# Performance work log

Measured on AMD Instinct MI355X. Metric: run time of the kernel, lower is better.

Reference implementation:

```python
import jax, jax.numpy as jnp
import numpy as np

K = 32          # neighbors
HEAD_DIM = 8    # out_channels // num_heads = 64 // 8


def _ln(x, g, b, eps=1e-5):
    m = x.mean(-1, keepdims=True)
    v = ((x - m) ** 2).mean(-1, keepdims=True)
    return (x - m) * jax.lax.rsqrt(v + eps) * g + b


def _knn(x, k):
    # x: [B,N,3]; torch code takes top-k of NEGATIVE squared distance -> nearest
    sq = jnp.sum(x * x, axis=-1)                        # [B,N]
    inner = jnp.einsum('bnc,bmc->bnm', x, x)            # [B,N,N]
    neg_dist = -(sq[:, :, None] - 2.0 * inner + sq[:, None, :])
    return jax.lax.top_k(neg_dist, k)[1]                # [B,N,k]


def _gather(points, idx):
    # points: [B,M,C], idx: [B,N,K] -> [B,N,K,C]
    return jax.vmap(lambda p, i: p[i])(points, idx)


def _forward(xyz, features, ln1_g, ln1_b, Wq, bq, Wk, bk, Wv, bv,
             d_W1, d_b1, d_g, d_b, d_W2, d_b2,
             g_W1, g_b1, g_g, g_b, g_W2, g_b2,
             Wo, bo, ln2_g, ln2_b, ca_W1, ca_b1, ca_W2, ca_b2, ln3_g, ln3_b):
    fn = _ln(features, ln1_g, ln1_b)                    # norm1
    idx = _knn(xyz, K)                                  # [B,N,K]
    nxyz = _gather(xyz, idx)                            # [B,N,K,3]
    nfeat = _gather(fn, idx)                            # [B,N,K,C]
    pos_diff = xyz[:, :, None, :] - nxyz                # [B,N,K,3]
    # fc_delta: Linear -> LN -> ReLU -> Linear
    pe = jax.nn.relu(_ln(pos_diff @ d_W1 + d_b1, d_g, d_b)) @ d_W2 + d_b2
    q = (fn @ Wq + bq)[:, :, None, :]                   # [B,N,1,C]
    k = nfeat @ Wk + bk                                 # [B,N,K,C]
    v = nfeat @ Wv + bv
    # head permutes in torch are identity reshapes; vector attention in [B,N,K,C]
    attn_in = q - k + pe
    a = jax.nn.relu(_ln(attn_in @ g_W1 + g_b1, g_g, g_b)) @ g_W2 + g_b2
    a = jax.nn.softmax(a / np.sqrt(HEAD_DIM).astype(np.float32), axis=2)
    out = jnp.sum(a * (v + pe), axis=2)                 # [B,N,C]
    out = _ln(out @ Wo + bo, ln2_g, ln2_b)              # fc_out + norm2
    cw = jax.nn.sigmoid(jax.nn.relu(out.mean(axis=1) @ ca_W1 + ca_b1) @ ca_W2 + ca_b2)
    out = _ln(out * cw[:, None, :], ln3_g, ln3_b)       # channel attn + norm3
    return out + features                               # in==out -> no skip_proj


def setup_inputs() -> dict:
    key = jax.random.key(0)
    ks = jax.random.split(key, 12)
    B, N, C = 2, 8192, 64
    s = 1.0 / np.sqrt(C)
    w = lambda k, shape, sc: jax.random.normal(k, shape, jnp.float32) * sc
    return dict(
        xyz=jax.random.normal(ks[0], (B, N, 3), jnp.float32),
        features=jax.random.normal(ks[1], (B, N, C), jnp.float32),
        ln1_g=jnp.ones(C), ln1_b=jnp.zeros(C),
        Wq=w(ks[2], (C, C), s), bq=jnp.zeros(C),
        Wk=w(ks[3], (C, C), s), bk=jnp.zeros(C),
        Wv=w(ks[4], (C, C), s), bv=jnp.zeros(C),
        d_W1=w(ks[5], (3, C), 1.0 / np.sqrt(3)), d_b1=jnp.zeros(C),
        d_g=jnp.ones(C), d_b=jnp.zeros(C),
        d_W2=w(ks[6], (C, C), s), d_b2=jnp.zeros(C),
        g_W1=w(ks[7], (C, C), s), g_b1=jnp.zeros(C),
        g_g=jnp.ones(C), g_b=jnp.zeros(C),
        g_W2=w(ks[8], (C, C), s), g_b2=jnp.zeros(C),
        Wo=w(ks[9], (C, C), s), bo=jnp.zeros(C),
        ln2_g=jnp.ones(C), ln2_b=jnp.zeros(C),
        ca_W1=w(ks[10], (C, C // 4), s), ca_b1=jnp.zeros(C // 4),
        ca_W2=w(ks[11], (C // 4, C), 1.0 / np.sqrt(C // 4)), ca_b2=jnp.zeros(C),
        ln3_g=jnp.ones(C), ln3_b=jnp.zeros(C),
    )


def reference(xyz, features, ln1_g, ln1_b, Wq, bq, Wk, bk, Wv, bv,
              d_W1, d_b1, d_g, d_b, d_W2, d_b2,
              g_W1, g_b1, g_g, g_b, g_W2, g_b2,
              Wo, bo, ln2_g, ln2_b, ca_W1, ca_b1, ca_W2, ca_b2, ln3_g, ln3_b):
    return _forward(xyz, features, ln1_g, ln1_b, Wq, bq, Wk, bk, Wv, bv,
                    d_W1, d_b1, d_g, d_b, d_W2, d_b2,
                    g_W1, g_b1, g_g, g_b, g_W2, g_b2,
                    Wo, bo, ln2_g, ln2_b, ca_W1, ca_b1, ca_W2, ca_b2, ln3_g, ln3_b)
```

## Files before the change

### kernel.cpp

```cpp
#include <hip/hip_runtime.h>

static constexpr int gB = 2;
static constexpr int gN = 8192;
static constexpr int gC = 64;
static constexpr int gK = 32;

using u16 = unsigned short;
using u32 = unsigned int;
using u64 = unsigned long long;

__device__ __forceinline__ float wsum(float v) {
#pragma unroll
    for (int m = 32; m; m >>= 1) v += __shfl_xor(v, m, 64);
    return v;
}

__device__ __forceinline__ u16 f2bf(float f) {
    u32 u = __float_as_uint(f);
    return (u16)((u + 0x7FFFu + ((u >> 16) & 1u)) >> 16);
}
__device__ __forceinline__ float bf2f(u16 v) {
    return __uint_as_float(((u32)v) << 16);
}

__global__ __launch_bounds__(256) void k_lnqkv(
    const float* __restrict__ feat, const float* __restrict__ ln1g, const float* __restrict__ ln1b,
    const float* __restrict__ Wq, const float* __restrict__ bq,
    const float* __restrict__ Wk, const float* __restrict__ bk,
    const float* __restrict__ Wv, const float* __restrict__ bv,
    float* __restrict__ Qo, float* __restrict__ Ko, float* __restrict__ Vo,
    float* __restrict__ zero_region)
{
    if (blockIdx.x == 0) zero_region[threadIdx.x] = 0.f;
    int wave = threadIdx.x >> 6, lane = threadIdx.x & 63;
    int p = blockIdx.x * 4 + wave;
    float x = feat[(size_t)p * gC + lane];
    float mu = wsum(x) * (1.f / 64);
    float d = x - mu;
    float var = wsum(d * d) * (1.f / 64);
    float inv = 1.f / sqrtf(var + 1e-5f);
    float fn = d * inv * ln1g[lane] + ln1b[lane];
    float qa = bq[lane], ka = bk[lane], va = bv[lane];
    for (int cp = 0; cp < 64; ++cp) {
        float hv = __shfl(fn, cp, 64);
        qa += hv * Wq[cp * 64 + lane];
        ka += hv * Wk[cp * 64 + lane];
        va += hv * Wv[cp * 64 + lane];
    }
    size_t o = (size_t)p * gC + lane;
    Qo[o] = qa; Ko[o] = ka; Vo[o] = va;
}

__global__ __launch_bounds__(64) void k_knn(const float* __restrict__ xyz, int* __restrict__ idxo)
{
#pragma clang fp contract(off)
    int lane = threadIdx.x;
    int q = blockIdx.x;
    int b = q >> 13;
    int n = q & (gN - 1);
    const float* base = xyz + (size_t)b * gN * 3;
    float xi = base[n * 3 + 0];
    float yi = base[n * 3 + 1];
    float zi = base[n * 3 + 2];
    float ni_ = sqrtf((xi * xi + yi * yi) + zi * zi);
    float sqi = ni_ * ni_;
    u64 lst[10];
#pragma unroll
    for (int e = 0; e < 10; ++e) lst[e] = 0ull;
    for (int jj = 0; jj < 128; ++jj) {
        int j = (jj << 6) | lane;
        float x = base[j * 3 + 0];
        float y = base[j * 3 + 1];
        float z = base[j * 3 + 2];
        float nj_ = sqrtf((x * x + y * y) + z * z);
        float sqj = nj_ * nj_;
        float inner = (xi * x + yi * y) + zi * z;
        float nd = -((sqi - 2.0f * inner) + sqj);
        u32 u = __float_as_uint(nd);
        u32 kh = u ^ (0x80000000u | (u32)((int)u >> 31));
        u64 pk = ((u64)kh << 32) | (u32)(8191 - j);
        if (pk > lst[9]) {
            lst[9] = pk;
#pragma unroll
            for (int e = 9; e > 0; --e) {
                if (lst[e] > lst[e - 1]) { u64 t = lst[e - 1]; lst[e - 1] = lst[e]; lst[e] = t; }
            }
        }
    }
    int* op = idxo + (size_t)q * gK;
    for (int r = 0; r < gK; ++r) {
        u64 g = lst[0];
#pragma unroll
        for (int m = 32; m; m >>= 1) {
            u64 o = __shfl_xor(g, m, 64);
            g = (o > g) ? o : g;
        }
        if (lst[0] == g) {
#pragma unroll
            for (int e = 0; e < 9; ++e) lst[e] = lst[e + 1];
            lst[9] = 0ull;
        }
        if (lane == 0) op[r] = 8191 - (int)(g & 0x1FFFu);
    }
}

__global__ __launch_bounds__(64, 2) void k_attn(
    const float* __restrict__ xyz,
    const float* __restrict__ Qb, const float* __restrict__ Kb, const float* __restrict__ Vb,
    const int* __restrict__ idxi,
    const float* __restrict__ dW1, const float* __restrict__ db1,
    const float* __restrict__ dgv, const float* __restrict__ dbv,
    const float* __restrict__ dW2, const float* __restrict__ db2,
    const float* __restrict__ gW1, const float* __restrict__ gb1,
    const float* __restrict__ ggv, const float* __restrict__ gbv,
    const float* __restrict__ gW2, const float* __restrict__ gb2,
    float* __restrict__ att)
{
    __shared__ u16 actb[64][64];
    __shared__ u16 peb[64][64];
    __shared__ float qlds[2][64];
    int lane = threadIdx.x;
    int half = lane >> 5;
    int kk = lane & 31;
    int pA = blockIdx.x * 2;
    int p = pA + half;
    int b = p >> 13;

    qlds[0][lane] = Qb[(size_t)pA * gC + lane];
    qlds[1][lane] = Qb[(size_t)(pA + 1) * gC + lane];
    __syncthreads();

    int j = idxi[(size_t)p * gK + kk];
    const float* xp = xyz + (size_t)p * 3;
    const float* xj = xyz + ((size_t)b * gN + j) * 3;
    float dx = xp[0] - xj[0];
    float dy = xp[1] - xj[1];
    float dz = xp[2] - xj[2];

    float acc[64];

#pragma unroll
    for (int c = 0; c < 64; ++c)
        acc[c] = dx * dW1[c] + dy * dW1[64 + c] + dz * dW1[128 + c] + db1[c];

    {
        float s0 = 0, s1 = 0, s2 = 0, s3 = 0;
#pragma unroll
        for (int c = 0; c < 64; c += 4) { s0 += acc[c]; s1 += acc[c + 1]; s2 += acc[c + 2]; s3 += acc[c + 3]; }
        float mu = ((s0 + s1) + (s2 + s3)) * (1.f / 64);
        float v0 = 0, v1 = 0, v2 = 0, v3 = 0;
#pragma unroll
        for (int c = 0; c < 64; c += 4) {
            acc[c] -= mu; acc[c + 1] -= mu; acc[c + 2] -= mu; acc[c + 3] -= mu;
            v0 += acc[c] * acc[c]; v1 += acc[c + 1] * acc[c + 1];
            v2 += acc[c + 2] * acc[c + 2]; v3 += acc[c + 3] * acc[c + 3];
        }
        float var = ((v0 + v1) + (v2 + v3)) * (1.f / 64);
        float inv = 1.f / sqrtf(var + 1e-5f);
#pragma unroll
        for (int c = 0; c < 64; ++c)
            actb[c][lane] = f2bf(fmaxf(acc[c] * inv * dgv[c] + dbv[c], 0.f));
    }

#pragma unroll
    for (int c = 0; c < 64; ++c) acc[c] = db2[c];
    for (int cp = 0; cp < 64; ++cp) {
        float h = bf2f(actb[cp][lane]);
#pragma unroll
        for (int c = 0; c < 64; ++c) acc[c] += h * dW2[cp * 64 + c];
    }
#pragma unroll
    for (int c = 0; c < 64; ++c) peb[c][lane] = f2bf(acc[c]);

    {
        const float* Kj = Kb + ((size_t)b * gN + j) * gC;
#pragma unroll
        for (int c4 = 0; c4 < 16; ++c4) {
            float4 kv = reinterpret_cast<const float4*>(Kj)[c4];
            int c = c4 * 4;
            actb[c + 0][lane] = f2bf((qlds[half][c + 0] - kv.x) + acc[c + 0]);
            actb[c + 1][lane] = f2bf((qlds[half][c + 1] - kv.y) + acc[c + 1]);
            actb[c + 2][lane] = f2bf((qlds[half][c + 2] - kv.z) + acc[c + 2]);
            actb[c + 3][lane] = f2bf((qlds[half][c + 3] - kv.w) + acc[c + 3]);
        }
    }

#pragma unroll
    for (int c = 0; c < 64; ++c) acc[c] = gb1[c];
    for (int cp = 0; cp < 64; ++cp) {
        float h = bf2f(actb[cp][lane]);
#pragma unroll
        for (int c = 0; c < 64; ++c) acc[c] += h * gW1[cp * 64 + c];
    }
    {
        float s0 = 0, s1 = 0, s2 = 0, s3 = 0;
#pragma unroll
        for (int c = 0; c < 64; c += 4) { s0 += acc[c]; s1 += acc[c + 1]; s2 += acc[c + 2]; s3 += acc[c + 3]; }
        float mu = ((s0 + s1) + (s2 + s3)) * (1.f / 64);
        float v0 = 0, v1 = 0, v2 = 0, v3 = 0;
#pragma unroll
        for (int c = 0; c < 64; c += 4) {
            acc[c] -= mu; acc[c + 1] -= mu; acc[c + 2] -= mu; acc[c + 3] -= mu;
            v0 += acc[c] * acc[c]; v1 += acc[c + 1] * acc[c + 1];
            v2 += acc[c + 2] * acc[c + 2]; v3 += acc[c + 3] * acc[c + 3];
        }
        float var = ((v0 + v1) + (v2 + v3)) * (1.f / 64);
        float inv = 1.f / sqrtf(var + 1e-5f);
#pragma unroll
        for (int c = 0; c < 64; ++c)
            actb[c][lane] = f2bf(fmaxf(acc[c] * inv * ggv[c] + gbv[c], 0.f));
    }

#pragma unroll
    for (int c = 0; c < 64; ++c) acc[c] = gb2[c];
    for (int cp = 0; cp < 64; ++cp) {
        float h = bf2f(actb[cp][lane]);
#pragma unroll
        for (int c = 0; c < 64; ++c) acc[c] += h * gW2[cp * 64 + c];
    }
#pragma unroll
    for (int c = 0; c < 64; ++c)
        acc[c] = acc[c] * 0.3535533905932738f;

    {
        const float* Vj = Vb + ((size_t)b * gN + j) * gC;
        float* op = att + (size_t)p * gC;
        for (int c4 = 0; c4 < 16; ++c4) {
            float4 vv4 = reinterpret_cast<const float4*>(Vj)[c4];
            float vva[4] = {vv4.x, vv4.y, vv4.z, vv4.w};
#pragma unroll
            for (int i = 0; i < 4; ++i) {
                int c = c4 * 4 + i;
                float l = acc[c];
                float gm = l;
#pragma unroll
                for (int m = 16; m; m >>= 1) gm = fmaxf(gm, __shfl_xor(gm, m, 64));
                float e = expf(l - gm);
                float w = e * (vva[i] + bf2f(peb[c][lane]));
                float se = e, sw = w;
#pragma unroll
                for (int m = 16; m; m >>= 1) {
                    se += __shfl_xor(se, m, 64);
                    sw += __shfl_xor(sw, m, 64);
                }
                if (kk == (c & 31)) op[c] = sw / se;
            }
        }
    }
}

__global__ __launch_bounds__(256) void k_out(
    float* __restrict__ att,
    const float* __restrict__ Wo, const float* __restrict__ bo,
    const float* __restrict__ ln2g, const float* __restrict__ ln2b,
    float* __restrict__ meanb)
{
    __shared__ __align__(16) float hb[4][64];
    int lane = threadIdx.x & 63;
    int p = blockIdx.x * 4 + (threadIdx.x >> 6);
    int b = p >> 13;
    float* hbuf = hb[threadIdx.x >> 6];
    float wo[64];
#pragma unroll
    for (int r = 0; r < 64; ++r) wo[r] = Wo[r * 64 + lane];
    float x = att[(size_t)p * gC + lane];
    hbuf[lane] = x;
    float acc = bo[lane];
#pragma unroll
    for (int q4 = 0; q4 < 16; ++q4) {
        float4 hq = *reinterpret_cast<const float4*>(&hbuf[q4 * 4]);
        acc += hq.x * wo[q4 * 4 + 0] + hq.y * wo[q4 * 4 + 1]
             + hq.z * wo[q4 * 4 + 2] + hq.w * wo[q4 * 4 + 3];
    }
    float mu = wsum(acc) * (1.f / 64);
    float d = acc - mu;
    float var = wsum(d * d) * (1.f / 64);
    float inv = 1.f / sqrtf(var + 1e-5f);
    float y = d * inv * ln2g[lane] + ln2b[lane];
    att[(size_t)p * gC + lane] = y;
    atomicAdd(&meanb[b * 64 + lane], y * (1.f / gN));
}

__global__ void k_cw(const float* __restrict__ meanb,
                     const float* __restrict__ caW1, const float* __restrict__ cab1,
                     const float* __restrict__ caW2, const float* __restrict__ cab2,
                     float* __restrict__ cw)
{
    int b = blockIdx.x, lane = threadIdx.x;
    float mv = meanb[b * 64 + lane];
    float hj = (lane < 16) ? cab1[lane] : 0.f;
    for (int cp = 0; cp < 64; ++cp) {
        float mcp = __shfl(mv, cp, 64);
        if (lane < 16) hj += mcp * caW1[cp * 16 + lane];
    }
    hj = fmaxf(hj, 0.f);
    float acc = cab2[lane];
    for (int jj = 0; jj < 16; ++jj) {
        float hv = __shfl(hj, jj, 64);
        acc += hv * caW2[jj * 64 + lane];
    }
    cw[b * 64 + lane] = 1.f / (1.f + expf(-acc));
}

__global__ __launch_bounds__(256) void k_final(
    const float* __restrict__ out2, const float* __restrict__ cw,
    const float* __restrict__ ln3g, const float* __restrict__ ln3b,
    const float* __restrict__ feat, float* __restrict__ outp)
{
    int lane = threadIdx.x & 63;
    int p = blockIdx.x * 4 + (threadIdx.x >> 6);
    int b = p >> 13;
    float x = out2[(size_t)p * gC + lane] * cw[b * 64 + lane];
    float mu = wsum(x) * (1.f / 64);
    float d = x - mu;
    float var = wsum(d * d) * (1.f / 64);
    float inv = 1.f / sqrtf(var + 1e-5f);
    float y = d * inv * ln3g[lane] + ln3b[lane];
    outp[(size_t)p * gC + lane] = y + feat[(size_t)p * gC + lane];
}

extern "C" void kernel_launch(void* const* d_in, const int* in_sizes, int n_in,
                              void* d_out, int out_size, void* d_ws, size_t ws_size,
                              hipStream_t stream)
{
    (void)in_sizes; (void)n_in; (void)out_size; (void)ws_size;
    const float* xyz  = (const float*)d_in[0];
    const float* feat = (const float*)d_in[1];
    const float* ln1g = (const float*)d_in[2];
    const float* ln1b = (const float*)d_in[3];
    const float* Wq   = (const float*)d_in[4];
    const float* bq   = (const float*)d_in[5];
    const float* Wk   = (const float*)d_in[6];
    const float* bk   = (const float*)d_in[7];
    const float* Wv   = (const float*)d_in[8];
    const float* bv   = (const float*)d_in[9];
    const float* dW1  = (const float*)d_in[10];
    const float* db1  = (const float*)d_in[11];
    const float* dg   = (const float*)d_in[12];
    const float* db   = (const float*)d_in[13];
    const float* dW2  = (const float*)d_in[14];
    const float* db2  = (const float*)d_in[15];
    const float* gW1  = (const float*)d_in[16];
    const float* gb1  = (const float*)d_in[17];
    const float* gg   = (const float*)d_in[18];
    const float* gb   = (const float*)d_in[19];
    const float* gW2  = (const float*)d_in[20];
    const float* gb2  = (const float*)d_in[21];
    const float* Wo   = (const float*)d_in[22];
    const float* bo   = (const float*)d_in[23];
    const float* ln2g = (const float*)d_in[24];
    const float* ln2b = (const float*)d_in[25];
    const float* caW1 = (const float*)d_in[26];
    const float* cab1 = (const float*)d_in[27];
    const float* caW2 = (const float*)d_in[28];
    const float* cab2 = (const float*)d_in[29];
    const float* ln3g = (const float*)d_in[30];
    const float* ln3b = (const float*)d_in[31];

    const size_t BNC = (size_t)gB * gN * gC;
    float* Q    = (float*)d_ws;
    float* Kt   = Q + BNC;
    float* Vt   = Kt + BNC;
    float* att  = Vt + BNC;
    int*   idx  = (int*)(att + BNC);
    float* meanb = (float*)(idx + (size_t)gB * gN * gK);
    float* cw    = meanb + 128;

    const int PB = (gB * gN) / 4;

    k_lnqkv<<<PB, 256, 0, stream>>>(feat, ln1g, ln1b, Wq, bq, Wk, bk, Wv, bv, Q, Kt, Vt, meanb);
    k_knn<<<gB * gN, 64, 0, stream>>>(xyz, idx);
    k_attn<<<(gB * gN) / 2, 64, 0, stream>>>(xyz, Q, Kt, Vt, idx,
                                             dW1, db1, dg, db, dW2, db2,
                                             gW1, gb1, gg, gb, gW2, gb2, att);
    k_out<<<PB, 256, 0, stream>>>(att, Wo, bo, ln2g, ln2b, meanb);
    k_cw<<<gB, 64, 0, stream>>>(meanb, caW1, cab1, caW2, cab2, cw);
    k_final<<<PB, 256, 0, stream>>>(att, cw, ln3g, ln3b, feat, (float*)d_out);
}
```

Measured before the change: 1.178 ms.

## Remap attention kernel to lane-per-channel with LDS-staged bf16 weights

```diff
diff --git a/kernel.cpp b/kernel.cpp
--- a/kernel.cpp
+++ b/kernel.cpp
@@ -104,7 +104,7 @@
     }
 }
 
-__global__ __launch_bounds__(64, 2) void k_attn(
+__global__ __launch_bounds__(256, 2) void k_attn(
     const float* __restrict__ xyz,
     const float* __restrict__ Qb, const float* __restrict__ Kb, const float* __restrict__ Vb,
     const int* __restrict__ idxi,
@@ -116,136 +116,133 @@
     const float* __restrict__ gW2, const float* __restrict__ gb2,
     float* __restrict__ att)
 {
-    __shared__ u16 actb[64][64];
-    __shared__ u16 peb[64][64];
-    __shared__ float qlds[2][64];
-    int lane = threadIdx.x;
-    int half = lane >> 5;
-    int kk = lane & 31;
-    int pA = blockIdx.x * 2;
-    int p = pA + half;
+    __shared__ u16 wd2s[64 * 64];
+    __shared__ u16 wg1s[64 * 64];
+    __shared__ u16 wg2s[64 * 64];
+    __shared__ float hbuf[4][32][64];
+    __shared__ u16 pebuf[4][32][64];
+    __shared__ float4 dxb[4][32];
+    __shared__ int jb[4][32];
+
+    int tid = threadIdx.x;
+    int w = tid >> 6, lane = tid & 63;
+    int p = blockIdx.x * 4 + w;
     int b = p >> 13;
 
-    qlds[0][lane] = Qb[(size_t)pA * gC + lane];
-    qlds[1][lane] = Qb[(size_t)(pA + 1) * gC + lane];
+    for (int i = tid; i < 4096; i += 256) {
+        int cp = i >> 6, c = i & 63;
+        int di = c * 64 + ((((cp >> 2) ^ (c & 15)) << 2) | (cp & 3));
+        wd2s[di] = f2bf(dW2[i]);
+        wg1s[di] = f2bf(gW1[i]);
+        wg2s[di] = f2bf(gW2[i]);
+    }
+    if (lane < 32) {
+        int j = idxi[(size_t)p * gK + lane];
+        jb[w][lane] = j;
+        const float* xp = xyz + (size_t)p * 3;
+        const float* xj = xyz + ((size_t)b * gN + j) * 3;
+        dxb[w][lane] = make_float4(xp[0] - xj[0], xp[1] - xj[1], xp[2] - xj[2], 0.f);
+    }
     __syncthreads();
 
-    int j = idxi[(size_t)p * gK + kk];
-    const float* xp = xyz + (size_t)p * 3;
-    const float* xj = xyz + ((size_t)b * gN + j) * 3;
-    float dx = xp[0] - xj[0];
-    float dy = xp[1] - xj[1];
-    float dz = xp[2] - xj[2];
-
-    float acc[64];
-
-#pragma unroll
-    for (int c = 0; c < 64; ++c)
-        acc[c] = dx * dW1[c] + dy * dW1[64 + c] + dz * dW1[128 + c] + db1[c];
+    float w1x = dW1[lane], w1y = dW1[64 + lane], w1z = dW1[128 + lane], vb1 = db1[lane];
+    float vdg = dgv[lane], vdb = dbv[lane];
+    float vb2 = db2[lane];
+    float vg1b = gb1[lane], vgg = ggv[lane], vgb = gbv[lane], vg2b = gb2[lane];
+    float q = Qb[(size_t)p * gC + lane];
+
+#pragma unroll
+    for (int kk = 0; kk < 32; ++kk) {
+        float4 d4 = dxb[w][kk];
+        float t = d4.x * w1x + d4.y * w1y + d4.z * w1z + vb1;
+        float mu = wsum(t) * (1.f / 64);
+        float td = t - mu;
+        float var = wsum(td * td) * (1.f / 64);
+        float inv = 1.f / sqrtf(var + 1e-5f);
+        hbuf[w][kk][lane] = fmaxf(td * inv * vdg + vdb, 0.f);
+    }
+
+    float acc[32];
+
+#pragma unroll
+    for (int kk = 0; kk < 32; ++kk) acc[kk] = vb2;
+    for (int cp4 = 0; cp4 < 16; ++cp4) {
+        int pg = cp4 ^ (lane & 15);
+        uint2 wp = *reinterpret_cast<const uint2*>(&wd2s[lane * 64 + pg * 4]);
+        float w0 = bf2f((u16)(wp.x & 0xFFFFu)), w1 = bf2f((u16)(wp.x >> 16));
+        float w2 = bf2f((u16)(wp.y & 0xFFFFu)), w3 = bf2f((u16)(wp.y >> 16));
+#pragma unroll
+        for (int kk = 0; kk < 32; ++kk) {
+            float4 h4 = *reinterpret_cast<const float4*>(&hbuf[w][kk][cp4 * 4]);
+            acc[kk] += h4.x * w0 + h4.y * w1 + h4.z * w2 + h4.w * w3;
+        }
+    }
+#pragma unroll
+    for (int kk = 0; kk < 32; ++kk) pebuf[w][kk][lane] = f2bf(acc[kk]);
 
     {
-        float s0 = 0, s1 = 0, s2 = 0, s3 = 0;
-#pragma unroll
-        for (int c = 0; c < 64; c += 4) { s0 += acc[c]; s1 += acc[c + 1]; s2 += acc[c + 2]; s3 += acc[c + 3]; }
-        float mu = ((s0 + s1) + (s2 + s3)) * (1.f / 64);
-        float v0 = 0, v1 = 0, v2 = 0, v3 = 0;
-#pragma unroll
-        for (int c = 0; c < 64; c += 4) {
-            acc[c] -= mu; acc[c + 1] -= mu; acc[c + 2] -= mu; acc[c + 3] -= mu;
-            v0 += acc[c] * acc[c]; v1 += acc[c + 1] * acc[c + 1];
-            v2 += acc[c + 2] * acc[c + 2]; v3 += acc[c + 3] * acc[c + 3];
-        }
-        float var = ((v0 + v1) + (v2 + v3)) * (1.f / 64);
+        const float* Kbb = Kb + (size_t)b * gN * gC;
+#pragma unroll
+        for (int kk = 0; kk < 32; ++kk) {
+            float kv = Kbb[(size_t)jb[w][kk] * gC + lane];
+            hbuf[w][kk][lane] = (q - kv) + acc[kk];
+        }
+    }
+
+#pragma unroll
+    for (int kk = 0; kk < 32; ++kk) acc[kk] = vg1b;
+    for (int cp4 = 0; cp4 < 16; ++cp4) {
+        int pg = cp4 ^ (lane & 15);
+        uint2 wp = *reinterpret_cast<const uint2*>(&wg1s[lane * 64 + pg * 4]);
+        float w0 = bf2f((u16)(wp.x & 0xFFFFu)), w1 = bf2f((u16)(wp.x >> 16));
+        float w2 = bf2f((u16)(wp.y & 0xFFFFu)), w3 = bf2f((u16)(wp.y >> 16));
+#pragma unroll
+        for (int kk = 0; kk < 32; ++kk) {
+            float4 h4 = *reinterpret_cast<const float4*>(&hbuf[w][kk][cp4 * 4]);
+            acc[kk] += h4.x * w0 + h4.y * w1 + h4.z * w2 + h4.w * w3;
+        }
+    }
+#pragma unroll
+    for (int kk = 0; kk < 32; ++kk) {
+        float a = acc[kk];
+        float mu = wsum(a) * (1.f / 64);
+        float ad = a - mu;
+        float var = wsum(ad * ad) * (1.f / 64);
         float inv = 1.f / sqrtf(var + 1e-5f);
-#pragma unroll
-        for (int c = 0; c < 64; ++c)
-            actb[c][lane] = f2bf(fmaxf(acc[c] * inv * dgv[c] + dbv[c], 0.f));
-    }
-
-#pragma unroll
-    for (int c = 0; c < 64; ++c) acc[c] = db2[c];
-    for (int cp = 0; cp < 64; ++cp) {
-        float h = bf2f(actb[cp][lane]);
-#pragma unroll
-        for (int c = 0; c < 64; ++c) acc[c] += h * dW2[cp * 64 + c];
-    }
-#pragma unroll
-    for (int c = 0; c < 64; ++c) peb[c][lane] = f2bf(acc[c]);
-
+        hbuf[w][kk][lane] = fmaxf(ad * inv * vgg + vgb, 0.f);
+    }
+
+#pragma unroll
+    for (int kk = 0; kk < 32; ++kk) acc[kk] = vg2b;
+    for (int cp4 = 0; cp4 < 16; ++cp4) {
+        int pg = cp4 ^ (lane & 15);
+        uint2 wp = *reinterpret_cast<const uint2*>(&wg2s[lane * 64 + pg * 4]);
+        float w0 = bf2f((u16)(wp.x & 0xFFFFu)), w1 = bf2f((u16)(wp.x >> 16));
+        float w2 = bf2f((u16)(wp.y & 0xFFFFu)), w3 = bf2f((u16)(wp.y >> 16));
+#pragma unroll
+        for (int kk = 0; kk < 32; ++kk) {
+            float4 h4 = *reinterpret_cast<const float4*>(&hbuf[w][kk][cp4 * 4]);
+            acc[kk] += h4.x * w0 + h4.y * w1 + h4.z * w2 + h4.w * w3;
+        }
+    }
+
+#pragma unroll
+    for (int kk = 0; kk < 32; ++kk) acc[kk] *= 0.3535533905932738f;
+    float mx = acc[0];
+#pragma unroll
+    for (int kk = 1; kk < 32; ++kk) mx = fmaxf(mx, acc[kk]);
+    float s = 0.f;
+#pragma unroll
+    for (int kk = 0; kk < 32; ++kk) { acc[kk] = expf(acc[kk] - mx); s += acc[kk]; }
     {
-        const float* Kj = Kb + ((size_t)b * gN + j) * gC;
-#pragma unroll
-        for (int c4 = 0; c4 < 16; ++c4) {
-            float4 kv = reinterpret_cast<const float4*>(Kj)[c4];
-            int c = c4 * 4;
-            actb[c + 0][lane] = f2bf((qlds[half][c + 0] - kv.x) + acc[c + 0]);
-            actb[c + 1][lane] = f2bf((qlds[half][c + 1] - kv.y) + acc[c + 1]);
-            actb[c + 2][lane] = f2bf((qlds[half][c + 2] - kv.z) + acc[c + 2]);
-            actb[c + 3][lane] = f2bf((qlds[half][c + 3] - kv.w) + acc[c + 3]);
-        }
-    }
-
-#pragma unroll
-    for (int c = 0; c < 64; ++c) acc[c] = gb1[c];
-    for (int cp = 0; cp < 64; ++cp) {
-        float h = bf2f(actb[cp][lane]);
-#pragma unroll
-        for (int c = 0; c < 64; ++c) acc[c] += h * gW1[cp * 64 + c];
-    }
-    {
-        float s0 = 0, s1 = 0, s2 = 0, s3 = 0;
-#pragma unroll
-        for (int c = 0; c < 64; c += 4) { s0 += acc[c]; s1 += acc[c + 1]; s2 += acc[c + 2]; s3 += acc[c + 3]; }
-        float mu = ((s0 + s1) + (s2 + s3)) * (1.f / 64);
-        float v0 = 0, v1 = 0, v2 = 0, v3 = 0;
-#pragma unroll
-        for (int c = 0; c < 64; c += 4) {
-            acc[c] -= mu; acc[c + 1] -= mu; acc[c + 2] -= mu; acc[c + 3] -= mu;
-            v0 += acc[c] * acc[c]; v1 += acc[c + 1] * acc[c + 1];
-            v2 += acc[c + 2] * acc[c + 2]; v3 += acc[c + 3] * acc[c + 3];
-        }
-        float var = ((v0 + v1) + (v2 + v3)) * (1.f / 64);
-        float inv = 1.f / sqrtf(var + 1e-5f);
-#pragma unroll
-        for (int c = 0; c < 64; ++c)
-            actb[c][lane] = f2bf(fmaxf(acc[c] * inv * ggv[c] + gbv[c], 0.f));
-    }
-
-#pragma unroll
-    for (int c = 0; c < 64; ++c) acc[c] = gb2[c];
-    for (int cp = 0; cp < 64; ++cp) {
-        float h = bf2f(actb[cp][lane]);
-#pragma unroll
-        for (int c = 0; c < 64; ++c) acc[c] += h * gW2[cp * 64 + c];
-    }
-#pragma unroll
-    for (int c = 0; c < 64; ++c)
-        acc[c] = acc[c] * 0.3535533905932738f;
-
-    {
-        const float* Vj = Vb + ((size_t)b * gN + j) * gC;
-        float* op = att + (size_t)p * gC;
-        for (int c4 = 0; c4 < 16; ++c4) {
-            float4 vv4 = reinterpret_cast<const float4*>(Vj)[c4];
-            float vva[4] = {vv4.x, vv4.y, vv4.z, vv4.w};
-#pragma unroll
-            for (int i = 0; i < 4; ++i) {
-                int c = c4 * 4 + i;
-                float l = acc[c];
-                float gm = l;
-#pragma unroll
-                for (int m = 16; m; m >>= 1) gm = fmaxf(gm, __shfl_xor(gm, m, 64));
-                float e = expf(l - gm);
-                float w = e * (vva[i] + bf2f(peb[c][lane]));
-                float se = e, sw = w;
-#pragma unroll
-                for (int m = 16; m; m >>= 1) {
-                    se += __shfl_xor(se, m, 64);
-                    sw += __shfl_xor(sw, m, 64);
-                }
-                if (kk == (c & 31)) op[c] = sw / se;
-            }
-        }
+        const float* Vbb = Vb + (size_t)b * gN * gC;
+        float o = 0.f;
+#pragma unroll
+        for (int kk = 0; kk < 32; ++kk) {
+            float vv = Vbb[(size_t)jb[w][kk] * gC + lane];
+            o += acc[kk] * (vv + bf2f(pebuf[w][kk][lane]));
+        }
+        att[(size_t)p * gC + lane] = o / s;
     }
 }
 
@@ -370,9 +367,9 @@
 
     k_lnqkv<<<PB, 256, 0, stream>>>(feat, ln1g, ln1b, Wq, bq, Wk, bk, Wv, bv, Q, Kt, Vt, meanb);
     k_knn<<<gB * gN, 64, 0, stream>>>(xyz, idx);
-    k_attn<<<(gB * gN) / 2, 64, 0, stream>>>(xyz, Q, Kt, Vt, idx,
-                                             dW1, db1, dg, db, dW2, db2,
-                                             gW1, gb1, gg, gb, gW2, gb2, att);
+    k_attn<<<PB, 256, 0, stream>>>(xyz, Q, Kt, Vt, idx,
+                                   dW1, db1, dg, db, dW2, db2,
+                                   gW1, gb1, gg, gb, gW2, gb2, att);
     k_out<<<PB, 256, 0, stream>>>(att, Wo, bo, ln2g, ln2b, meanb);
     k_cw<<<gB, 64, 0, stream>>>(meanb, caW1, cab1, caW2, cab2, cw);
     k_final<<<PB, 256, 0, stream>>>(att, cw, ln3g, ln3b, feat, (float*)d_out);
```

Result: faster. 1.108 ms (-5.9%).
